# Performance work log

Hardware: AMD Instinct MI355X
Metric: run time of the kernel (lower is better)

Reference implementation:

```python
import jax, jax.numpy as jnp
import numpy as np

N = 100000      # nodes
E = 3200000     # edges
F_IN = 64       # num_input_features
HID = 3         # hardcoded hidden width in GCN
F_OUT = 256     # gcn_output_features
F_TR = 512      # transformer_feature_size


def setup_inputs() -> dict:
    key = jax.random.key(0)
    ks = jax.random.split(key, 12)
    x = jax.random.normal(ks[0], (N, F_IN), dtype=jnp.float32)
    edge_index = jax.random.randint(ks[1], (2, E), 0, N, dtype=jnp.int64)
    s = 0.05
    # ChebConv1 (K=2): two weight mats [in,out] + bias
    W0a = jax.random.normal(ks[2], (F_IN, HID), jnp.float32) * s
    W1a = jax.random.normal(ks[3], (F_IN, HID), jnp.float32) * s
    b1 = jax.random.normal(ks[4], (HID,), jnp.float32) * s
    # ChebConv2 (K=2)
    W0b = jax.random.normal(ks[5], (HID, F_OUT), jnp.float32) * s
    W1b = jax.random.normal(ks[6], (HID, F_OUT), jnp.float32) * s
    b2 = jax.random.normal(ks[7], (F_OUT,), jnp.float32) * s
    # final Linear
    Wl = jax.random.normal(ks[8], (F_OUT, F_TR), jnp.float32) * s
    bl = jax.random.normal(ks[9], (F_TR,), jnp.float32) * s
    return {"x": x, "edge_index": edge_index, "W0a": W0a, "W1a": W1a,
            "b1": b1, "W0b": W0b, "W1b": W1b, "b2": b2, "Wl": Wl, "bl": bl}


def _cheb_norm(edge_index, num_nodes):
    # PyG ChebConv.__norm__ with sym normalization, lambda_max=2.0:
    # L_hat = 2L/2 - I = -D^{-1/2} A D^{-1/2} (diagonal cancels to 0).
    src, dst = edge_index[0], edge_index[1]
    w = jnp.where(src != dst, 1.0, 0.0).astype(jnp.float32)  # remove_self_loops
    deg = jnp.zeros((num_nodes,), jnp.float32).at[src].add(w)
    dinv = jnp.where(deg > 0, jax.lax.rsqrt(jnp.maximum(deg, 1.0)), 0.0)
    return -dinv[src] * w * dinv[dst]  # [E]


def _cheb_conv(x, edge_index, norm, W0, W1, b):
    # K=2 Chebyshev: Tx0 = x, Tx1 = L_hat @ x (scatter-add over edges)
    src, dst = edge_index[0], edge_index[1]
    Tx1 = jnp.zeros_like(x).at[dst].add(norm[:, None] * x[src])
    return x @ W0 + Tx1 @ W1 + b


def reference(x, edge_index, W0a, W1a, b1, W0b, W1b, b2, Wl, bl):
    norm = _cheb_norm(edge_index, x.shape[0])
    h = jax.nn.relu(_cheb_conv(x, edge_index, norm, W0a, W1a, b1))
    h = jax.nn.relu(_cheb_conv(h, edge_index, norm, W0b, W1b, b2))
    return h @ Wl + bl
```

## Files before the change

### kernel.cpp

```cpp
#include <hip/hip_runtime.h>
#include <hip/hip_bf16.h>


#define MAXNB 1024
#define BSH 7
#define BSZ 128
#define SRC_BITS 20
#define SRC_MASK ((1u << SRC_BITS) - 1u)
#define EPB 16384

typedef __attribute__((ext_vector_type(8))) short short8;
typedef __attribute__((ext_vector_type(4))) float f32x4;

static __device__ inline unsigned short f2bf(float f) {
    union { float f; unsigned u; } v; v.f = f;
    unsigned r = (v.u + 0x7fffu + ((v.u >> 16) & 1u)) >> 16;
    return (unsigned short)r;
}

__global__ __launch_bounds__(256) void k_prep(const float* __restrict__ Wl,
                                              unsigned short* __restrict__ WlT,
                                              unsigned* __restrict__ subcurD,
                                              unsigned* __restrict__ subcurS) {
    __shared__ float tile[32][33];
    int t = threadIdx.x, tx = t & 31, ty = t >> 5;
    if (blockIdx.x == 0) {
        for (int i = t; i < MAXNB; i += 256) { subcurD[i] = 0u; subcurS[i] = 0u; }
    }
    int kb = (blockIdx.x & 7) * 32;
    int cb = (blockIdx.x >> 3) * 32;
#pragma unroll
    for (int r = 0; r < 4; r++) {
        int k = kb + ty + r * 8;
        tile[ty + r * 8][tx] = Wl[(size_t)k * 512 + cb + tx];
    }
    __syncthreads();
#pragma unroll
    for (int r = 0; r < 4; r++) {
        int c = cb + ty + r * 8;
        WlT[(size_t)c * 256 + kb + tx] = f2bf(tile[tx][ty + r * 8]);
    }
}

__global__ __launch_bounds__(1024) void k_hist(const int* __restrict__ ei, int E, int NB,
                                               unsigned* __restrict__ subcurD,
                                               unsigned* __restrict__ subcurS,
                                               unsigned* __restrict__ baseD,
                                               unsigned* __restrict__ baseS) {
    __shared__ unsigned hD[MAXNB], hS[MAXNB];
    int t = threadIdx.x, blk = blockIdx.x;
    for (int i = t; i < NB; i += 1024) { hD[i] = 0u; hS[i] = 0u; }
    __syncthreads();
    int e0 = blk * EPB, e1 = min(e0 + EPB, E);
    for (int e = e0 + t; e < e1; e += 1024) {
        int s = ei[e], d = ei[E + e];
        if (s != d) {
            atomicAdd(&hD[d >> BSH], 1u);
            atomicAdd(&hS[s >> BSH], 1u);
        }
    }
    __syncthreads();
    unsigned* bD = baseD + (size_t)blk * NB;
    unsigned* bS = baseS + (size_t)blk * NB;
    for (int i = t; i < NB; i += 1024) {
        unsigned h = hD[i];
        if (h) bD[i] = atomicAdd(&subcurD[i], h);
        h = hS[i];
        if (h) bS[i] = atomicAdd(&subcurS[i], h);
    }
}

__global__ __launch_bounds__(1024) void k_scan(const unsigned* __restrict__ totD,
                                               const unsigned* __restrict__ totS,
                                               unsigned* __restrict__ startD,
                                               unsigned* __restrict__ startS, int NB) {
    __shared__ unsigned a[MAXNB], b[MAXNB];
    int t = threadIdx.x;
    for (int i = t; i < NB; i += 1024) a[i] = totD[i];
    __syncthreads();
    unsigned* s = a; unsigned* d = b;
    for (int off = 1; off < NB; off <<= 1) {
        for (int i = t; i < NB; i += 1024)
            d[i] = s[i] + (i >= off ? s[i - off] : 0u);
        __syncthreads();
        unsigned* tmp = s; s = d; d = tmp;
    }
    for (int i = t; i < NB; i += 1024)
        startD[i] = (i == 0) ? 0u : s[i - 1];
    if (t == 0) startD[NB] = s[NB - 1];
    __syncthreads();
    for (int i = t; i < NB; i += 1024) a[i] = totS[i];
    __syncthreads();
    s = a; d = b;
    for (int off = 1; off < NB; off <<= 1) {
        for (int i = t; i < NB; i += 1024)
            d[i] = s[i] + (i >= off ? s[i - off] : 0u);
        __syncthreads();
        unsigned* tmp = s; s = d; d = tmp;
    }
    for (int i = t; i < NB; i += 1024)
        startS[i] = (i == 0) ? 0u : s[i - 1];
    if (t == 0) startS[NB] = s[NB - 1];
}

__global__ __launch_bounds__(1024) void k_place(const int* __restrict__ ei, int E, int NB,
                                                const unsigned* __restrict__ startD,
                                                const unsigned* __restrict__ startS,
                                                const unsigned* __restrict__ baseD,
                                                const unsigned* __restrict__ baseS,
                                                unsigned* __restrict__ dstbin,
                                                unsigned char* __restrict__ srcbin) {
    __shared__ unsigned oD[MAXNB], oS[MAXNB], cD[MAXNB], cS[MAXNB];
    int t = threadIdx.x, blk = blockIdx.x;
    const unsigned* bD = baseD + (size_t)blk * NB;
    const unsigned* bS = baseS + (size_t)blk * NB;
    for (int i = t; i < NB; i += 1024) {
        oD[i] = startD[i] + bD[i];
        oS[i] = startS[i] + bS[i];
        cD[i] = 0u; cS[i] = 0u;
    }
    __syncthreads();
    int e0 = blk * EPB, e1 = min(e0 + EPB, E);
    for (int e = e0 + t; e < e1; e += 1024) {
        int s = ei[e], d = ei[E + e];
        if (s != d) {
            int bk = d >> BSH;
            unsigned pos = oD[bk] + atomicAdd(&cD[bk], 1u);
            dstbin[pos] = ((unsigned)(d & (BSZ - 1)) << SRC_BITS) | (unsigned)s;
            int bs = s >> BSH;
            unsigned ps = oS[bs] + atomicAdd(&cS[bs], 1u);
            srcbin[ps] = (unsigned char)(s & (BSZ - 1));
        }
    }
}

__global__ __launch_bounds__(256) void k_sortdeg(
    const unsigned* __restrict__ dstbin, const unsigned* __restrict__ startD,
    unsigned* __restrict__ dsorted, unsigned* __restrict__ nodeoff,
    const unsigned char* __restrict__ srcbin, const unsigned* __restrict__ startS,
    const float* __restrict__ x, const float* __restrict__ W0a,
    const float* __restrict__ W1a, float* __restrict__ dinv,
    float4* __restrict__ a3v, float4* __restrict__ y3v, int N) {
    __shared__ unsigned cnt[BSZ], tmp[BSZ], cur[BSZ];
    __shared__ unsigned cnt4[4][BSZ];
    __shared__ float w0[192], w1[192];
    __shared__ float dl[BSZ];
    int t = threadIdx.x, b = blockIdx.x;
    if (t < 192) { w0[t] = W0a[t]; w1[t] = W1a[t]; }
    if (t < BSZ) cnt[t] = 0u;
    for (int i = t; i < 4 * BSZ; i += 256) ((unsigned*)cnt4)[i] = 0u;
    __syncthreads();
    unsigned d0 = startD[b], d1 = startD[b + 1];
    for (unsigned e = d0 + t; e < d1; e += 256)
        atomicAdd(&cnt[dstbin[e] >> SRC_BITS], 1u);
    unsigned s0 = startS[b], s1 = startS[b + 1];
    int rep = t & 3;
    for (unsigned i = s0 + t; i < s1; i += 256) atomicAdd(&cnt4[rep][srcbin[i]], 1u);
    __syncthreads();
    for (int off = 1; off < BSZ; off <<= 1) {
        if (t < BSZ) tmp[t] = cnt[t] + (t >= off ? cnt[t - off] : 0u);
        __syncthreads();
        if (t < BSZ) cnt[t] = tmp[t];
        __syncthreads();
    }
    if (t <= BSZ) {
        unsigned ex = (t == 0) ? 0u : cnt[t - 1];
        int idx = b * BSZ + t;
        if (idx <= N) nodeoff[idx] = d0 + ex;
        if (t < BSZ) cur[t] = ex;
    }
    __syncthreads();
    for (unsigned e = d0 + t; e < d1; e += 256) {
        unsigned p = dstbin[e];
        unsigned pos = d0 + atomicAdd(&cur[p >> SRC_BITS], 1u);
        dsorted[pos] = p & SRC_MASK;
    }
    if (t < BSZ) {
        unsigned c = cnt4[0][t] + cnt4[1][t] + cnt4[2][t] + cnt4[3][t];
        float dv = c ? rsqrtf((float)c) : 0.f;
        dl[t] = dv;
        int g = b * BSZ + t;
        if (g < N) dinv[g] = dv;
    }
    __syncthreads();
    int q = t & 3;
#pragma unroll
    for (int pass = 0; pass < 2; pass++) {
        int nn = (t >> 2) + pass * 64;
        int node = b * BSZ + nn;
        float acc[6] = {0.f, 0.f, 0.f, 0.f, 0.f, 0.f};
        if (node < N) {
            const float4* xr = (const float4*)(x + (size_t)node * 64 + q * 16);
#pragma unroll
            for (int i = 0; i < 4; i++) {
                float4 v = xr[i];
                float xs[4] = {v.x, v.y, v.z, v.w};
#pragma unroll
                for (int c = 0; c < 4; c++) {
                    int f = q * 16 + i * 4 + c;
                    float xi = xs[c];
                    acc[0] += xi * w0[f * 3 + 0];
                    acc[1] += xi * w0[f * 3 + 1];
                    acc[2] += xi * w0[f * 3 + 2];
                    acc[3] += xi * w1[f * 3 + 0];
                    acc[4] += xi * w1[f * 3 + 1];
                    acc[5] += xi * w1[f * 3 + 2];
                }
            }
        }
#pragma unroll
        for (int m = 1; m < 4; m <<= 1)
#pragma unroll
            for (int j = 0; j < 6; j++) acc[j] += __shfl_xor(acc[j], m, 64);
        if (q == 0 && node < N) {
            a3v[node] = make_float4(acc[0], acc[1], acc[2], 0.f);
            y3v[node] = make_float4(acc[3], acc[4], acc[5], dl[nn]);
        }
    }
}

__global__ __launch_bounds__(512) void k_tgather(
    const unsigned* __restrict__ dsorted, const unsigned* __restrict__ nodeoff,
    const float4* __restrict__ v4, const float* __restrict__ dinv,
    const float4* __restrict__ a3v, const float* __restrict__ b1,
    float4* __restrict__ outv, int N, int phase) {
    int t = threadIdx.x;
    int g = t >> 3, q = t & 7;
    int node = blockIdx.x * 64 + g;
    if (node >= N) return;
    float dv = dinv[node];
    unsigned o0 = nodeoff[node], o1 = nodeoff[node + 1];
    float s0 = 0.f, s1 = 0.f, s2 = 0.f;
    for (unsigned e = o0 + q; e < o1; e += 8) {
        float4 v = v4[dsorted[e]];
        float nm = -v.w * dv;
        s0 += nm * v.x; s1 += nm * v.y; s2 += nm * v.z;
    }
#pragma unroll
    for (int m = 1; m < 8; m <<= 1) {
        s0 += __shfl_xor(s0, m, 64);
        s1 += __shfl_xor(s1, m, 64);
        s2 += __shfl_xor(s2, m, 64);
    }
    if (q == 0) {
        if (phase == 1) {
            float4 a = a3v[node];
            outv[node] = make_float4(fmaxf(s0 + a.x + b1[0], 0.f),
                                     fmaxf(s1 + a.y + b1[1], 0.f),
                                     fmaxf(s2 + a.z + b1[2], 0.f), dv);
        } else {
            outv[node] = make_float4(s0, s1, s2, 0.f);
        }
    }
}

__global__ __launch_bounds__(256) void k_final_mfma(
    const float4* __restrict__ h1v, const float4* __restrict__ t2r,
    const float* __restrict__ W0b, const float* __restrict__ W1b,
    const float* __restrict__ b2, const unsigned short* __restrict__ WlT,
    const float* __restrict__ bl, float* __restrict__ out, int N) {
    __shared__ unsigned short h2s[64 * 256];
    __shared__ float4 u4[64][2];
    char* h2b = (char*)h2s;
    int t = threadIdx.x, b = blockIdx.x;
    int n0 = b * 64;

    if (t < 64) {
        int g = n0 + t;
        u4[t][0] = (g < N) ? h1v[g] : make_float4(0.f, 0.f, 0.f, 0.f);
    } else if (t < 128) {
        int g = n0 + t - 64;
        u4[t - 64][1] = (g < N) ? t2r[g] : make_float4(0.f, 0.f, 0.f, 0.f);
    }
    __syncthreads();

    {
        int k0 = (t & 127) * 2;
        int rh = (t >> 7) * 32;
        float w00a = W0b[k0],       w00b = W0b[k0 + 1];
        float w01a = W0b[256 + k0], w01b = W0b[256 + k0 + 1];
        float w02a = W0b[512 + k0], w02b = W0b[512 + k0 + 1];
        float w10a = W1b[k0],       w10b = W1b[k0 + 1];
        float w11a = W1b[256 + k0], w11b = W1b[256 + k0 + 1];
        float w12a = W1b[512 + k0], w12b = W1b[512 + k0 + 1];
        float bka = b2[k0], bkb = b2[k0 + 1];
        int kbyte = k0 * 2;
#pragma unroll
        for (int r = 0; r < 32; r++) {
            int rr = rh + r;
            float4 h = u4[rr][0];
            float4 v = u4[rr][1];
            float za = bka + h.x * w00a + h.y * w01a + h.z * w02a
                           + v.x * w10a + v.y * w11a + v.z * w12a;
            float zb = bkb + h.x * w00b + h.y * w01b + h.z * w02b
                           + v.x * w10b + v.y * w11b + v.z * w12b;
            za = fmaxf(za, 0.f); zb = fmaxf(zb, 0.f);
            unsigned pk = ((unsigned)f2bf(zb) << 16) | (unsigned)f2bf(za);
            int byte = rr * 512 + (kbyte ^ ((rr & 7) << 4));
            *(unsigned*)(h2b + byte) = pk;
        }
    }
    __syncthreads();

    int w = t >> 6, l = t & 63;
    int col0 = w * 128;
    int lrow = l & 15, lkb = (l >> 4) * 8, cq = (l >> 4) * 4;

#pragma unroll
    for (int ch = 0; ch < 2; ch++) {
        int cb0 = col0 + ch * 64;
        f32x4 acc[4][4];
#pragma unroll
        for (int rt = 0; rt < 4; rt++)
#pragma unroll
            for (int ct = 0; ct < 4; ct++) acc[rt][ct] = (f32x4)0.f;

#pragma unroll
        for (int ks = 0; ks < 8; ks++) {
            int kel = ks * 32 + lkb;
            short8 af[4];
#pragma unroll
            for (int rt = 0; rt < 4; rt++) {
                int r = rt * 16 + lrow;
                int byte = r * 512 + ((kel * 2) ^ ((r & 7) << 4));
                af[rt] = *(const short8*)(h2b + byte);
            }
            short8 bf[4];
#pragma unroll
            for (int ct = 0; ct < 4; ct++) {
                int c = cb0 + ct * 16 + lrow;
                bf[ct] = *(const short8*)(WlT + (size_t)c * 256 + kel);
            }
#pragma unroll
            for (int rt = 0; rt < 4; rt++)
#pragma unroll
                for (int ct = 0; ct < 4; ct++)
                    acc[rt][ct] = __builtin_amdgcn_mfma_f32_16x16x32_bf16(
                        bf[ct], af[rt], acc[rt][ct], 0, 0, 0);
        }

        f32x4 blv[4];
#pragma unroll
        for (int ct = 0; ct < 4; ct++)
            blv[ct] = *(const f32x4*)(bl + cb0 + ct * 16 + cq);
#pragma unroll
        for (int rt = 0; rt < 4; rt++) {
            int row = n0 + rt * 16 + lrow;
            if (row < N) {
                float* orow = out + (size_t)row * 512 + cb0 + cq;
#pragma unroll
                for (int ct = 0; ct < 4; ct++) {
                    f32x4 sv = acc[rt][ct] + blv[ct];
                    __builtin_nontemporal_store(sv, (f32x4*)(orow + ct * 16));
                }
            }
        }
    }
}

extern "C" void kernel_launch(void* const* d_in, const int* in_sizes, int n_in,
                              void* d_out, int out_size, void* d_ws, size_t ws_size,
                              hipStream_t stream) {
    const float* x   = (const float*)d_in[0];
    const int*   ei  = (const int*)d_in[1];
    const float* W0a = (const float*)d_in[2];
    const float* W1a = (const float*)d_in[3];
    const float* b1  = (const float*)d_in[4];
    const float* W0b = (const float*)d_in[5];
    const float* W1b = (const float*)d_in[6];
    const float* b2  = (const float*)d_in[7];
    const float* Wl  = (const float*)d_in[8];
    const float* bl  = (const float*)d_in[9];
    float* out = (float*)d_out;

    const int N = in_sizes[0] / 64;
    const int E = in_sizes[1] / 2;
    const int NB = (N + BSZ - 1) >> BSH;
    const int CB = (E + EPB - 1) / EPB;
    const int NB64 = (N + 63) / 64;

    char* base = (char*)d_ws;
    size_t off = 0;
    auto alloc = [&](size_t bytes) {
        void* p = base + off;
        off = (off + bytes + 255) & ~(size_t)255;
        return p;
    };
    unsigned* subcurD = (unsigned*)alloc(MAXNB * 4);
    unsigned* subcurS = (unsigned*)alloc(MAXNB * 4);
    unsigned* startD  = (unsigned*)alloc((MAXNB + 1) * 4);
    unsigned* startS  = (unsigned*)alloc((MAXNB + 1) * 4);
    unsigned* baseD   = (unsigned*)alloc((size_t)CB * NB * 4);
    unsigned* baseS   = (unsigned*)alloc((size_t)CB * NB * 4);
    unsigned* dstbin  = (unsigned*)alloc((size_t)E * 4);
    unsigned* dsorted = (unsigned*)alloc((size_t)E * 4);
    unsigned* nodeoff = (unsigned*)alloc((size_t)(N + 1) * 4);
    unsigned char* srcbin = (unsigned char*)alloc((size_t)E);
    float* dinv = (float*)alloc((size_t)N * 4);
    float* a3v  = (float*)alloc((size_t)N * 16);
    float* y3v  = (float*)alloc((size_t)N * 16);
    float* h1v  = (float*)alloc((size_t)N * 16);
    float* t2r  = (float*)alloc((size_t)N * 16);
    unsigned short* WlT = (unsigned short*)alloc(512 * 256 * 2);

    k_prep<<<128, 256, 0, stream>>>(Wl, WlT, subcurD, subcurS);
    k_hist<<<CB, 1024, 0, stream>>>(ei, E, NB, subcurD, subcurS, baseD, baseS);
    k_scan<<<1, 1024, 0, stream>>>(subcurD, subcurS, startD, startS, NB);
    k_place<<<CB, 1024, 0, stream>>>(ei, E, NB, startD, startS, baseD, baseS,
                                     dstbin, srcbin);
    k_sortdeg<<<NB, 256, 0, stream>>>(dstbin, startD, dsorted, nodeoff,
                                      srcbin, startS, x, W0a, W1a, dinv,
                                      (float4*)a3v, (float4*)y3v, N);
    k_tgather<<<NB64, 512, 0, stream>>>(dsorted, nodeoff, (const float4*)y3v, dinv,
                                        (const float4*)a3v, b1, (float4*)h1v, N, 1);
    k_tgather<<<NB64, 512, 0, stream>>>(dsorted, nodeoff, (const float4*)h1v, dinv,
                                        (const float4*)a3v, b1, (float4*)t2r, N, 2);
    k_final_mfma<<<NB64, 256, 0, stream>>>(
        (const float4*)h1v, (const float4*)t2r, W0b, W1b, b2, WlT, bl, out, N);
}
```

Before: 234.2 us.

## Fuse second-layer neighbor gather into final MFMA kernel and vectorize edge reads

Removes the second k_tgather launch by performing the layer-2 Laplacian gather inside k_final_mfma, with 4 lanes per node, and writing the result straight to shared memory. This drops the t2r intermediate buffer and one kernel launch. The histogram and placement kernels now load edge indices as int4 when E is divisible by 4. The trade-off is that the final kernel takes on latency-bound irregular gathers with fewer lanes per node, which may serialize before the MFMA phase.

```diff
diff --git a/kernel.cpp b/kernel.cpp
--- a/kernel.cpp
+++ b/kernel.cpp
@@ -52,11 +52,25 @@
     for (int i = t; i < NB; i += 1024) { hD[i] = 0u; hS[i] = 0u; }
     __syncthreads();
     int e0 = blk * EPB, e1 = min(e0 + EPB, E);
-    for (int e = e0 + t; e < e1; e += 1024) {
-        int s = ei[e], d = ei[E + e];
-        if (s != d) {
-            atomicAdd(&hD[d >> BSH], 1u);
-            atomicAdd(&hS[s >> BSH], 1u);
+    if ((E & 3) == 0) {
+        int nv = (e1 - e0) >> 2;
+        const int4* s4 = (const int4*)(ei + e0);
+        const int4* d4 = (const int4*)(ei + (size_t)E + e0);
+        for (int i = t; i < nv; i += 1024) {
+            int4 ss = s4[i], dd = d4[i];
+            if (ss.x != dd.x) { atomicAdd(&hD[dd.x >> BSH], 1u); atomicAdd(&hS[ss.x >> BSH], 1u); }
+            if (ss.y != dd.y) { atomicAdd(&hD[dd.y >> BSH], 1u); atomicAdd(&hS[ss.y >> BSH], 1u); }
+            if (ss.z != dd.z) { atomicAdd(&hD[dd.z >> BSH], 1u); atomicAdd(&hS[ss.z >> BSH], 1u); }
+            if (ss.w != dd.w) { atomicAdd(&hD[dd.w >> BSH], 1u); atomicAdd(&hS[ss.w >> BSH], 1u); }
+        }
+        for (int e = e0 + (nv << 2) + t; e < e1; e += 1024) {
+            int s = ei[e], d = ei[(size_t)E + e];
+            if (s != d) { atomicAdd(&hD[d >> BSH], 1u); atomicAdd(&hS[s >> BSH], 1u); }
+        }
+    } else {
+        for (int e = e0 + t; e < e1; e += 1024) {
+            int s = ei[e], d = ei[(size_t)E + e];
+            if (s != d) { atomicAdd(&hD[d >> BSH], 1u); atomicAdd(&hS[s >> BSH], 1u); }
         }
     }
     __syncthreads();
@@ -121,15 +135,49 @@
     }
     __syncthreads();
     int e0 = blk * EPB, e1 = min(e0 + EPB, E);
-    for (int e = e0 + t; e < e1; e += 1024) {
-        int s = ei[e], d = ei[E + e];
-        if (s != d) {
-            int bk = d >> BSH;
-            unsigned pos = oD[bk] + atomicAdd(&cD[bk], 1u);
-            dstbin[pos] = ((unsigned)(d & (BSZ - 1)) << SRC_BITS) | (unsigned)s;
-            int bs = s >> BSH;
-            unsigned ps = oS[bs] + atomicAdd(&cS[bs], 1u);
-            srcbin[ps] = (unsigned char)(s & (BSZ - 1));
+    if ((E & 3) == 0) {
+        int nv = (e1 - e0) >> 2;
+        const int4* s4 = (const int4*)(ei + e0);
+        const int4* d4 = (const int4*)(ei + (size_t)E + e0);
+        for (int i = t; i < nv; i += 1024) {
+            int4 ss = s4[i], dd = d4[i];
+            int sa[4] = {ss.x, ss.y, ss.z, ss.w};
+            int da[4] = {dd.x, dd.y, dd.z, dd.w};
+#pragma unroll
+            for (int j = 0; j < 4; j++) {
+                int s = sa[j], d = da[j];
+                if (s != d) {
+                    int bk = d >> BSH;
+                    unsigned pos = oD[bk] + atomicAdd(&cD[bk], 1u);
+                    dstbin[pos] = ((unsigned)(d & (BSZ - 1)) << SRC_BITS) | (unsigned)s;
+                    int bs = s >> BSH;
+                    unsigned ps = oS[bs] + atomicAdd(&cS[bs], 1u);
+                    srcbin[ps] = (unsigned char)(s & (BSZ - 1));
+                }
+            }
+        }
+        for (int e = e0 + (nv << 2) + t; e < e1; e += 1024) {
+            int s = ei[e], d = ei[(size_t)E + e];
+            if (s != d) {
+                int bk = d >> BSH;
+                unsigned pos = oD[bk] + atomicAdd(&cD[bk], 1u);
+                dstbin[pos] = ((unsigned)(d & (BSZ - 1)) << SRC_BITS) | (unsigned)s;
+                int bs = s >> BSH;
+                unsigned ps = oS[bs] + atomicAdd(&cS[bs], 1u);
+                srcbin[ps] = (unsigned char)(s & (BSZ - 1));
+            }
+        }
+    } else {
+        for (int e = e0 + t; e < e1; e += 1024) {
+            int s = ei[e], d = ei[(size_t)E + e];
+            if (s != d) {
+                int bk = d >> BSH;
+                unsigned pos = oD[bk] + atomicAdd(&cD[bk], 1u);
+                dstbin[pos] = ((unsigned)(d & (BSZ - 1)) << SRC_BITS) | (unsigned)s;
+                int bs = s >> BSH;
+                unsigned ps = oS[bs] + atomicAdd(&cS[bs], 1u);
+                srcbin[ps] = (unsigned char)(s & (BSZ - 1));
+            }
         }
     }
 }
@@ -223,7 +271,7 @@
     const unsigned* __restrict__ dsorted, const unsigned* __restrict__ nodeoff,
     const float4* __restrict__ v4, const float* __restrict__ dinv,
     const float4* __restrict__ a3v, const float* __restrict__ b1,
-    float4* __restrict__ outv, int N, int phase) {
+    float4* __restrict__ outv, int N) {
     int t = threadIdx.x;
     int g = t >> 3, q = t & 7;
     int node = blockIdx.x * 64 + g;
@@ -243,34 +291,54 @@
         s2 += __shfl_xor(s2, m, 64);
     }
     if (q == 0) {
-        if (phase == 1) {
-            float4 a = a3v[node];
-            outv[node] = make_float4(fmaxf(s0 + a.x + b1[0], 0.f),
-                                     fmaxf(s1 + a.y + b1[1], 0.f),
-                                     fmaxf(s2 + a.z + b1[2], 0.f), dv);
-        } else {
-            outv[node] = make_float4(s0, s1, s2, 0.f);
-        }
+        float4 a = a3v[node];
+        outv[node] = make_float4(fmaxf(s0 + a.x + b1[0], 0.f),
+                                 fmaxf(s1 + a.y + b1[1], 0.f),
+                                 fmaxf(s2 + a.z + b1[2], 0.f), dv);
     }
 }
 
 __global__ __launch_bounds__(256) void k_final_mfma(
-    const float4* __restrict__ h1v, const float4* __restrict__ t2r,
+    const float4* __restrict__ h1v, const unsigned* __restrict__ dsorted,
+    const unsigned* __restrict__ nodeoff,
     const float* __restrict__ W0b, const float* __restrict__ W1b,
     const float* __restrict__ b2, const unsigned short* __restrict__ WlT,
     const float* __restrict__ bl, float* __restrict__ out, int N) {
     __shared__ unsigned short h2s[64 * 256];
     __shared__ float4 u4[64][2];
+    __shared__ float dl[64];
     char* h2b = (char*)h2s;
     int t = threadIdx.x, b = blockIdx.x;
     int n0 = b * 64;
 
     if (t < 64) {
         int g = n0 + t;
-        u4[t][0] = (g < N) ? h1v[g] : make_float4(0.f, 0.f, 0.f, 0.f);
-    } else if (t < 128) {
-        int g = n0 + t - 64;
-        u4[t - 64][1] = (g < N) ? t2r[g] : make_float4(0.f, 0.f, 0.f, 0.f);
+        float4 hv = (g < N) ? h1v[g] : make_float4(0.f, 0.f, 0.f, 0.f);
+        u4[t][0] = hv;
+        dl[t] = hv.w;
+    }
+    __syncthreads();
+
+    {
+        int g = t >> 2, q = t & 3;
+        int node = n0 + g;
+        float s0 = 0.f, s1 = 0.f, s2 = 0.f;
+        if (node < N) {
+            float dv = dl[g];
+            unsigned o0 = nodeoff[node], o1 = nodeoff[node + 1];
+            for (unsigned e = o0 + q; e < o1; e += 4) {
+                float4 v = h1v[dsorted[e]];
+                float nm = -v.w * dv;
+                s0 += nm * v.x; s1 += nm * v.y; s2 += nm * v.z;
+            }
+        }
+#pragma unroll
+        for (int m = 1; m < 4; m <<= 1) {
+            s0 += __shfl_xor(s0, m, 64);
+            s1 += __shfl_xor(s1, m, 64);
+            s2 += __shfl_xor(s2, m, 64);
+        }
+        if (q == 0) u4[g][1] = make_float4(s0, s1, s2, 0.f);
     }
     __syncthreads();
 
@@ -400,7 +468,6 @@
     float* a3v  = (float*)alloc((size_t)N * 16);
     float* y3v  = (float*)alloc((size_t)N * 16);
     float* h1v  = (float*)alloc((size_t)N * 16);
-    float* t2r  = (float*)alloc((size_t)N * 16);
     unsigned short* WlT = (unsigned short*)alloc(512 * 256 * 2);
 
     k_prep<<<128, 256, 0, stream>>>(Wl, WlT, subcurD, subcurS);
@@ -412,9 +479,7 @@
                                       srcbin, startS, x, W0a, W1a, dinv,
                                       (float4*)a3v, (float4*)y3v, N);
     k_tgather<<<NB64, 512, 0, stream>>>(dsorted, nodeoff, (const float4*)y3v, dinv,
-                                        (const float4*)a3v, b1, (float4*)h1v, N, 1);
-    k_tgather<<<NB64, 512, 0, stream>>>(dsorted, nodeoff, (const float4*)h1v, dinv,
-                                        (const float4*)a3v, b1, (float4*)t2r, N, 2);
+                                        (const float4*)a3v, b1, (float4*)h1v, N);
     k_final_mfma<<<NB64, 256, 0, stream>>>(
-        (const float4*)h1v, (const float4*)t2r, W0b, W1b, b2, WlT, bl, out, N);
-}
+        (const float4*)h1v, dsorted, nodeoff, W0b, W1b, b2, WlT, bl, out, N);
+}
```

New measurement: 237.7 us. Within noise of the previous version (+1.5%).
